# Optimization experiments

Hardware: AMD Instinct MI355X
Metric: run time of the kernel (lower is better)

## Reference

```python
import jax, jax.numpy as jnp
import numpy as np


def _conv3x3(x, w, b):
    # NCHW conv, stride 1, pad 1
    y = jax.lax.conv_general_dilated(x, w, (1, 1), ((1, 1), (1, 1)),
                                     dimension_numbers=('NCHW', 'OIHW', 'NCHW'))
    return y + b[None, :, None, None]


def _deform_conv3x3(x, offset, w):
    # Deformable conv v1: 3x3, stride 1, pad 1, 1 deformable group, no bias.
    # offset: [B, 18, H, W] laid out as (dy_k, dx_k) for k = 0..8 (row-major taps).
    B, C, H, W = x.shape
    K = 9
    off = offset.reshape(B, K, 2, H, W)
    ky, kx = jnp.meshgrid(jnp.arange(3), jnp.arange(3), indexing='ij')
    ky = (ky.reshape(K) - 1).astype(x.dtype)  # kernel tap y-offset, pad=1
    kx = (kx.reshape(K) - 1).astype(x.dtype)
    hh = jnp.arange(H, dtype=x.dtype)
    ww = jnp.arange(W, dtype=x.dtype)
    # sampling locations [B, K, H, W]
    sy = hh[None, None, :, None] + ky[None, :, None, None] + off[:, :, 0]
    sx = ww[None, None, None, :] + kx[None, :, None, None] + off[:, :, 1]
    y0 = jnp.floor(sy)
    x0 = jnp.floor(sx)
    ly = sy - y0  # fractional parts
    lx = sx - x0
    x_flat = x.reshape(B, C, H * W)

    def gather(yi, xi, wgt):
        # zero-padding semantics: corners outside the image contribute 0
        valid = (yi >= 0) & (yi < H) & (xi >= 0) & (xi < W)
        idx = (jnp.clip(yi, 0, H - 1).astype(jnp.int32) * W
               + jnp.clip(xi, 0, W - 1).astype(jnp.int32)).reshape(B, 1, K * H * W)
        v = jnp.take_along_axis(x_flat, idx, axis=2).reshape(B, C, K, H, W)
        return v * (wgt * valid.astype(x.dtype))[:, None]

    sampled = (gather(y0,     x0,     (1 - ly) * (1 - lx))
             + gather(y0,     x0 + 1, (1 - ly) * lx)
             + gather(y0 + 1, x0,     ly * (1 - lx))
             + gather(y0 + 1, x0 + 1, ly * lx))  # [B, C, K, H, W]
    return jnp.einsum('bckhw,ock->bohw', sampled, w.reshape(w.shape[0], C, K))


def setup_inputs() -> dict:
    key = jax.random.key(0)
    ks = jax.random.split(key, 8)
    C, O = 256, 256
    return {
        'kernel': jax.random.normal(ks[0], (16, C, 16, 16), jnp.float32),
        'search': jax.random.normal(ks[1], (16, C, 32, 32), jnp.float32),
        'Toffset_w': jax.random.normal(ks[2], (18, C, 3, 3), jnp.float32) * 0.02,
        'Toffset_b': jnp.zeros((18,), jnp.float32),
        'Tdeform_w': jax.random.normal(ks[3], (O, C, 3, 3), jnp.float32) * 0.02,
        'Soffset_w': jax.random.normal(ks[4], (18, C, 3, 3), jnp.float32) * 0.02,
        'Soffset_b': jnp.zeros((18,), jnp.float32),
        'Sdeform_w': jax.random.normal(ks[5], (O, C, 3, 3), jnp.float32) * 0.02,
    }


def reference(kernel, search, Toffset_w, Toffset_b, Tdeform_w,
              Soffset_w, Soffset_b, Sdeform_w):
    kernel_offset = _conv3x3(kernel, Toffset_w, Toffset_b)
    kernel_out = _deform_conv3x3(kernel, kernel_offset, Tdeform_w)
    search_offset = _conv3x3(search, Soffset_w, Soffset_b)
    search_out = _deform_conv3x3(search, search_offset, Sdeform_w)
    return (kernel_out, search_out, kernel_offset, search_offset)
```

## Files before the change

### kernel.cpp

```cpp
#include <hip/hip_runtime.h>

#define CIN   256
#define OC    256
#define K_TOT 2304
#define CCH   32
#define NCHK  8
#define KCH   288
#define SSTR  296
#define DM    64

#define N_DW  (OC * K_TOT)
#define N_OW  (32 * K_TOT)
#define N_CVT (2 * N_DW + 2 * N_OW)
#define CVT_BLOCKS (N_CVT / 4 / 256)

typedef short  bf16x8 __attribute__((ext_vector_type(8)));
typedef float  f32x4  __attribute__((ext_vector_type(4)));
typedef unsigned short ushort_t;

__device__ __forceinline__ ushort_t f2bf(float f) {
    unsigned u = __builtin_bit_cast(unsigned, f);
    u += 0x7fffu + ((u >> 16) & 1u);
    return (ushort_t)(u >> 16);
}
__device__ __forceinline__ float bf2f(short s) {
    return __builtin_bit_cast(float, ((unsigned)(unsigned short)s) << 16);
}

__global__ __launch_bounds__(256) void prep_k(
    const float* __restrict__ tdw, const float* __restrict__ sdw,
    const float* __restrict__ tow, const float* __restrict__ sow,
    const float* __restrict__ kin, const float* __restrict__ sin_,
    ushort_t* __restrict__ wk_d, ushort_t* __restrict__ ws_d,
    ushort_t* __restrict__ wk_o, ushort_t* __restrict__ ws_o,
    ushort_t* __restrict__ xt_k, ushort_t* __restrict__ xt_s)
{
    __shared__ ushort_t tile[64][264];

    if (blockIdx.x < CVT_BLOCKS) {
        const int i = (blockIdx.x * 256 + threadIdx.x) * 4;
        const float* src; ushort_t* dst; int j; bool offw = false;
        if (i < N_DW)                    { src = tdw; dst = wk_d; j = i; }
        else if (i < 2 * N_DW)           { src = sdw; dst = ws_d; j = i - N_DW; }
        else if (i < 2 * N_DW + N_OW)    { src = tow; dst = wk_o; j = i - 2 * N_DW; offw = true; }
        else                             { src = sow; dst = ws_o; j = i - 2 * N_DW - N_OW; offw = true; }
        const int oc = j / K_TOT;
        const int k  = j - oc * K_TOT;
        const int cc = k / KCH;
        const int r  = k - cc * KCH;
        const int tap = r >> 5;
        const int cl  = r & 31;
        ushort4 o4 = {0, 0, 0, 0};
        if (!offw || oc < 18) {
            const float* sp = &src[((size_t)oc * CIN + cc * 32 + cl) * 9 + tap];
            o4.x = f2bf(sp[0]); o4.y = f2bf(sp[9]); o4.z = f2bf(sp[18]); o4.w = f2bf(sp[27]);
        }
        *(ushort4*)&dst[j] = o4;
        return;
    }

    const int bx2 = blockIdx.x - CVT_BLOCKS;
    int H, W, b, px0; const float* x; ushort_t* xt;
    if (bx2 < 64) {
        H = 16; W = 16; x = kin; xt = xt_k;
        b = bx2 >> 2; px0 = (bx2 & 3) * 64;
    } else {
        int t2 = bx2 - 64;
        H = 32; W = 32; x = sin_; xt = xt_s;
        b = t2 >> 4; px0 = (t2 & 15) * 64;
    }
    const int HW = H * W;
    const int t = threadIdx.x, lane = t & 63, wv = t >> 6;
    const float* xb = x + (size_t)b * CIN * HW;

    for (int it = 0; it < 16; ++it) {
        const int ch = wv * 64 + it * 4 + (lane >> 4);
        const int pq = (lane & 15) * 4;
        float4 v = *(const float4*)&xb[(size_t)ch * HW + px0 + pq];
        tile[pq + 0][ch] = f2bf(v.x);
        tile[pq + 1][ch] = f2bf(v.y);
        tile[pq + 2][ch] = f2bf(v.z);
        tile[pq + 3][ch] = f2bf(v.w);
    }
    __syncthreads();
    for (int it = 0; it < 8; ++it) {
        const int px = it * 8 + wv * 2 + (lane >> 5);
        const int cg = (lane & 31) * 8;
        bf16x8 v = *(const bf16x8*)&tile[px][cg];
        *(bf16x8*)&xt[((size_t)b * HW + px0 + px) * 256 + cg] = v;
    }
}

__global__ __launch_bounds__(256, 2) void conv_gemm_k(
    const ushort_t* __restrict__ xt_k, const ushort_t* __restrict__ kwgt,
    const float* __restrict__ kbias, float* __restrict__ kout,
    const ushort_t* __restrict__ xt_s, const ushort_t* __restrict__ swgt,
    const float* __restrict__ sbias, float* __restrict__ sout)
{
    __shared__ float sred[3][4][2][64][4];

    int H, W, sh, b, px0;
    const ushort_t* xt; const ushort_t* wgt; const float* bias; float* out;
    if (blockIdx.x < 64) {
        H = 16; W = 16; sh = 4; xt = xt_k; wgt = kwgt; bias = kbias; out = kout;
        b = blockIdx.x >> 2; px0 = (blockIdx.x & 3) * 64;
    } else {
        int t2 = blockIdx.x - 64;
        H = 32; W = 32; sh = 5; xt = xt_s; wgt = swgt; bias = sbias; out = sout;
        b = t2 >> 4; px0 = (t2 & 15) * 64;
    }
    const int HW = H * W;
    const int t = threadIdx.x, lane = t & 63, kh = t >> 6;
    const int l15 = lane & 15;
    const int cg8 = (lane >> 4) * 8;
    const ushort_t* xtb = xt + (size_t)b * HW * 256;

    int h[4], wc[4];
#pragma unroll
    for (int mt = 0; mt < 4; ++mt) {
        const int px = px0 + mt * 16 + l15;
        h[mt]  = px >> sh;
        wc[mt] = px & (W - 1);
    }
    const ushort_t* wrow0 = wgt + (size_t)(l15)      * K_TOT + cg8;
    const ushort_t* wrow1 = wgt + (size_t)(16 + l15) * K_TOT + cg8;

    f32x4 acc[4][2] = {};
    for (int cc = kh * 2; cc < kh * 2 + 2; ++cc) {
        const int cb = cc * 32 + cg8;
#pragma unroll
        for (int ks = 0; ks < 9; ++ks) {
            const bf16x8 b0 = *(const bf16x8*)&wrow0[(size_t)cc * KCH + ks * 32];
            const bf16x8 b1 = *(const bf16x8*)&wrow1[(size_t)cc * KCH + ks * 32];
            const int dy = ks / 3 - 1, dx = ks % 3 - 1;
#pragma unroll
            for (int mt = 0; mt < 4; ++mt) {
                const int y  = h[mt] + dy;
                const int xx = wc[mt] + dx;
                const bool ok = ((unsigned)y < (unsigned)H) && ((unsigned)xx < (unsigned)W);
                bf16x8 a = {};
                if (ok) a = *(const bf16x8*)&xtb[(size_t)(((y << sh) + xx) * 256 + cb)];
                acc[mt][0] = __builtin_amdgcn_mfma_f32_16x16x32_bf16(a, b0, acc[mt][0], 0, 0, 0);
                acc[mt][1] = __builtin_amdgcn_mfma_f32_16x16x32_bf16(a, b1, acc[mt][1], 0, 0, 0);
            }
        }
    }

    if (kh > 0) {
#pragma unroll
        for (int mt = 0; mt < 4; ++mt)
#pragma unroll
            for (int nt = 0; nt < 2; ++nt)
                *(float4*)&sred[kh - 1][mt][nt][lane][0] = *(float4*)&acc[mt][nt];
    }
    __syncthreads();
    if (kh == 0) {
        const int prow = (lane >> 4) * 4;
#pragma unroll
        for (int nt = 0; nt < 2; ++nt) {
            const int oc = nt * 16 + l15;
            if (oc < 18) {
                const float bs = bias[oc];
#pragma unroll
                for (int mt = 0; mt < 4; ++mt) {
                    float4 r = *(float4*)&acc[mt][nt];
#pragma unroll
                    for (int q = 0; q < 3; ++q) {
                        const float4 o = *(const float4*)&sred[q][mt][nt][lane][0];
                        r.x += o.x; r.y += o.y; r.z += o.z; r.w += o.w;
                    }
                    r.x += bs; r.y += bs; r.z += bs; r.w += bs;
                    *(float4*)(out + ((size_t)b * 18 + oc) * HW + px0 + mt * 16 + prow) = r;
                }
            }
        }
    }
}

__device__ __forceinline__ void dcn_load4(
    bf16x8* c, const ushort_t* __restrict__ xtb, int4 id, int cb)
{
    c[0] = *(const bf16x8*)&xtb[(size_t)id.x * 256 + cb];
    c[1] = *(const bf16x8*)&xtb[(size_t)id.y * 256 + cb];
    c[2] = *(const bf16x8*)&xtb[(size_t)id.z * 256 + cb];
    c[3] = *(const bf16x8*)&xtb[(size_t)id.w * 256 + cb];
}
__device__ __forceinline__ void dcn_proc2(
    ushort_t* swb, int so, const bf16x8* c, float4 wt)
{
    bf16x8 r;
#pragma unroll
    for (int j = 0; j < 8; ++j) {
        const float v = wt.x * bf2f(c[0][j]) + wt.y * bf2f(c[1][j])
                      + wt.z * bf2f(c[2][j]) + wt.w * bf2f(c[3][j]);
        r[j] = (short)f2bf(v);
    }
    *(bf16x8*)&swb[so] = r;
}

__global__ __launch_bounds__(512, 4) void deform_gemm_k(
    const ushort_t* __restrict__ xt_k, const float* __restrict__ koffs,
    const ushort_t* __restrict__ kwgt, float* __restrict__ kout,
    const ushort_t* __restrict__ xt_s, const float* __restrict__ soffs,
    const ushort_t* __restrict__ swgt_, float* __restrict__ sout)
{
    __shared__ __align__(16) ushort_t smp[DM][SSTR];
    __shared__ __align__(16) int      sidx[DM][9][4];
    __shared__ __align__(16) float    swt [DM][9][4];

    int H, W, b, px0;
    const ushort_t* xt; const float* offs; const ushort_t* wgt; float* out;
    if (blockIdx.x < 64) {
        const int xcd = blockIdx.x & 7, i = blockIdx.x >> 3;
        H = 16; W = 16; xt = xt_k; offs = koffs; wgt = kwgt; out = kout;
        b = xcd + 8 * (i & 1); px0 = (i >> 1) * 64;
    } else {
        const int t2 = blockIdx.x - 64;
        const int xcd = t2 & 7, i = t2 >> 3;
        H = 32; W = 32; xt = xt_s; offs = soffs; wgt = swgt_; out = sout;
        b = xcd + 8 * (i & 1); px0 = (i >> 1) * 64;
    }
    const int HW = H * W;
    const int t = threadIdx.x, lane = t & 63, wv = t >> 6;

#pragma unroll
    for (int u = 0; u < 2; ++u) {
        const int s = t + u * 512;
        if (s < DM * 9) {
            const int p = s / 9, k = s - 9 * p;
            const int pix = px0 + p;
            const int h  = pix / W;
            const int wc = pix - h * W;
            const float* ob = offs + (size_t)b * 18 * HW;
            const float dy = ob[(2 * k    ) * HW + pix];
            const float dx = ob[(2 * k + 1) * HW + pix];
            const float sy = (float)(h  + k / 3 - 1) + dy;
            const float sx = (float)(wc + k % 3 - 1) + dx;
            const float y0f = floorf(sy), x0f = floorf(sx);
            const float ly = sy - y0f, lx = sx - x0f;
            const int y0 = (int)y0f, x0 = (int)x0f;
#pragma unroll
            for (int j = 0; j < 4; ++j) {
                const int yy = y0 + (j >> 1);
                const int xx = x0 + (j & 1);
                const bool ok = ((unsigned)yy < (unsigned)H) && ((unsigned)xx < (unsigned)W);
                sidx[p][k][j] = min(max(yy, 0), H - 1) * W + min(max(xx, 0), W - 1);
                const float wj = ((j >> 1) ? ly : 1.f - ly) * ((j & 1) ? lx : 1.f - lx);
                swt[p][k][j] = ok ? wj : 0.f;
            }
        }
    }
    __syncthreads();

    const ushort_t* xtb = xt + (size_t)b * HW * 256;
    const int l15 = lane & 15;
    const int cg8 = (lane >> 4) * 8;
    const int ocb = wv * 32;
    const bool live4 = (t < 256);

    const int g0  = t >> 2;
    const int cgE = (t & 3) * 8;
    int uso[5];
#pragma unroll
    for (int q = 0; q < 5; ++q) {
        const int g  = g0 + q * 128;
        const int px = g / 9, tap = g - 9 * px;
        uso[q] = px * SSTR + tap * 32 + (t & 3) * 8;
    }

    const ushort_t* wrow0 = wgt + (size_t)(ocb      + l15) * K_TOT + cg8;
    const ushort_t* wrow1 = wgt + (size_t)(ocb + 16 + l15) * K_TOT + cg8;
    ushort_t* smpb = &smp[0][0];
    const int4*   sidxF = (const int4*)  &sidx[0][0][0];
    const float4* swtF  = (const float4*)&swt [0][0][0];

    f32x4 acc[4][2] = {};

    for (int cc = 0; cc < NCHK; ++cc) {
        const int cb = cc * 32 + cgE;
        const size_t kg0 = (size_t)cc * KCH;

        bf16x8 cA[4], cB[4];
        float4 wA, wB;
        bf16x8 bq[2][2];
        { const int4 id = sidxF[g0];       wA = swtF[g0];       dcn_load4(cA, xtb, id, cb); }
        { const int4 id = sidxF[g0 + 128]; wB = swtF[g0 + 128]; dcn_load4(cB, xtb, id, cb); }
        bq[0][0] = *(const bf16x8*)&wrow0[kg0];
        bq[0][1] = *(const bf16x8*)&wrow1[kg0];

        dcn_proc2(smpb, uso[0], cA, wA);
        { const int4 id = sidxF[g0 + 256]; wA = swtF[g0 + 256]; dcn_load4(cA, xtb, id, cb); }
        dcn_proc2(smpb, uso[1], cB, wB);
        { const int4 id = sidxF[g0 + 384]; wB = swtF[g0 + 384]; dcn_load4(cB, xtb, id, cb); }
        dcn_proc2(smpb, uso[2], cA, wA);
        if (live4) { const int4 id = sidxF[g0 + 512]; wA = swtF[g0 + 512]; dcn_load4(cA, xtb, id, cb); }
        dcn_proc2(smpb, uso[3], cB, wB);
        if (live4) dcn_proc2(smpb, uso[4], cA, wA);

        asm volatile("s_waitcnt lgkmcnt(0)" ::: "memory");
        __builtin_amdgcn_sched_barrier(0);
        __builtin_amdgcn_s_barrier();
        __builtin_amdgcn_sched_barrier(0);

        __builtin_amdgcn_s_setprio(1);
#pragma unroll
        for (int ks = 0; ks < 9; ++ks) {
            if (ks < 8) {
                bq[(ks + 1) & 1][0] = *(const bf16x8*)&wrow0[kg0 + (size_t)(ks + 1) * 32];
                bq[(ks + 1) & 1][1] = *(const bf16x8*)&wrow1[kg0 + (size_t)(ks + 1) * 32];
            }
            bf16x8 a[4];
#pragma unroll
            for (int mt = 0; mt < 4; ++mt)
                a[mt] = *(const bf16x8*)&smp[mt * 16 + l15][ks * 32 + cg8];
#pragma unroll
            for (int mt = 0; mt < 4; ++mt) {
                acc[mt][0] = __builtin_amdgcn_mfma_f32_16x16x32_bf16(a[mt], bq[ks & 1][0], acc[mt][0], 0, 0, 0);
                acc[mt][1] = __builtin_amdgcn_mfma_f32_16x16x32_bf16(a[mt], bq[ks & 1][1], acc[mt][1], 0, 0, 0);
            }
        }
        __builtin_amdgcn_s_setprio(0);

        if (cc < NCHK - 1) {
            __builtin_amdgcn_sched_barrier(0);
            __builtin_amdgcn_s_barrier();
            __builtin_amdgcn_sched_barrier(0);
        }
    }

    const int prow = (lane >> 4) * 4;
#pragma unroll
    for (int mt = 0; mt < 4; ++mt) {
#pragma unroll
        for (int nt = 0; nt < 2; ++nt) {
            const int oc = ocb + nt * 16 + l15;
            float* op = out + ((size_t)b * OC + oc) * HW + px0 + mt * 16 + prow;
            *(float4*)op = *(float4*)&acc[mt][nt];
        }
    }
}

extern "C" void kernel_launch(void* const* d_in, const int* in_sizes, int n_in,
                              void* d_out, int out_size, void* d_ws, size_t ws_size,
                              hipStream_t stream) {
    const float* kin = (const float*)d_in[0];
    const float* sin_ = (const float*)d_in[1];
    const float* tow = (const float*)d_in[2];
    const float* tob = (const float*)d_in[3];
    const float* tdw = (const float*)d_in[4];
    const float* sow = (const float*)d_in[5];
    const float* sob = (const float*)d_in[6];
    const float* sdw = (const float*)d_in[7];

    float* out = (float*)d_out;
    float* out_k  = out;
    float* out_s  = out_k + (size_t)16 * 256 * 16 * 16;
    float* out_ko = out_s + (size_t)16 * 256 * 32 * 32;
    float* out_so = out_ko + (size_t)16 * 18 * 16 * 16;

    ushort_t* wk_d = (ushort_t*)d_ws;
    ushort_t* ws_d = wk_d + N_DW;
    ushort_t* wk_o = ws_d + N_DW;
    ushort_t* ws_o = wk_o + N_OW;
    ushort_t* xt_k = ws_o + N_OW;
    ushort_t* xt_s = xt_k + (size_t)16 * 256 * 256;

    prep_k<<<dim3(CVT_BLOCKS + 320), 256, 0, stream>>>(
        tdw, sdw, tow, sow, kin, sin_,
        wk_d, ws_d, wk_o, ws_o, xt_k, xt_s);

    conv_gemm_k<<<dim3(320), 256, 0, stream>>>(
        xt_k, wk_o, tob, out_ko, xt_s, ws_o, sob, out_so);

    deform_gemm_k<<<dim3(320), 512, 0, stream>>>(
        xt_k, out_ko, wk_d, out_k, xt_s, out_so, ws_d, out_s);
}
```

Measured before the change: 207.5 us.

## Split offset-conv K across 8 waves with branchless zero-row loads and XCD-aware mapping

The offset conv GEMM now runs 512 threads per block, so each of 8 waves handles one 32-channel chunk instead of two, and the partial sums are reduced through a larger shared buffer with a padded layout. Out-of-bounds taps now load from a zeroed 256-element row placed after xt_s instead of using a predicated load, which lets all four A loads be issued before the MFMAs. Blocks are remapped so consecutive block IDs spread batches across XCDs. This adds more wave parallelism and memory-level parallelism, at the cost of a bigger reduction step and more LDS.

```diff
diff --git a/kernel.cpp b/kernel.cpp
--- a/kernel.cpp
+++ b/kernel.cpp
@@ -13,6 +13,8 @@
 #define N_OW  (32 * K_TOT)
 #define N_CVT (2 * N_DW + 2 * N_OW)
 #define CVT_BLOCKS (N_CVT / 4 / 256)
+#define XT_K_ELEMS ((size_t)16 * 256 * 256)
+#define XT_S_ELEMS ((size_t)16 * 1024 * 256)
 
 typedef short  bf16x8 __attribute__((ext_vector_type(8)));
 typedef float  f32x4  __attribute__((ext_vector_type(4)));
@@ -36,6 +38,11 @@
     ushort_t* __restrict__ xt_k, ushort_t* __restrict__ xt_s)
 {
     __shared__ ushort_t tile[64][264];
+
+    if (blockIdx.x == 0 && threadIdx.x < 64) {
+        ushort4 z = {0, 0, 0, 0};
+        *(ushort4*)&xt_s[XT_S_ELEMS + (size_t)threadIdx.x * 4] = z;
+    }
 
     if (blockIdx.x < CVT_BLOCKS) {
         const int i = (blockIdx.x * 256 + threadIdx.x) * 4;
@@ -91,23 +98,27 @@
     }
 }
 
-__global__ __launch_bounds__(256, 2) void conv_gemm_k(
+__global__ __launch_bounds__(512, 2) void conv_gemm_k(
     const ushort_t* __restrict__ xt_k, const ushort_t* __restrict__ kwgt,
     const float* __restrict__ kbias, float* __restrict__ kout,
     const ushort_t* __restrict__ xt_s, const ushort_t* __restrict__ swgt,
     const float* __restrict__ sbias, float* __restrict__ sout)
 {
-    __shared__ float sred[3][4][2][64][4];
-
-    int H, W, sh, b, px0;
+    __shared__ float sred[7][64][36];
+
+    int H, W, sh, b, px0; int zrel;
     const ushort_t* xt; const ushort_t* wgt; const float* bias; float* out;
     if (blockIdx.x < 64) {
+        const int xcd = blockIdx.x & 7, i = blockIdx.x >> 3;
         H = 16; W = 16; sh = 4; xt = xt_k; wgt = kwgt; bias = kbias; out = kout;
-        b = blockIdx.x >> 2; px0 = (blockIdx.x & 3) * 64;
+        b = xcd + 8 * (i & 1); px0 = (i >> 1) * 64;
+        zrel = (int)(XT_K_ELEMS + XT_S_ELEMS - (size_t)b * 256 * 256);
     } else {
-        int t2 = blockIdx.x - 64;
+        const int t2 = blockIdx.x - 64;
+        const int xcd = t2 & 7, i = t2 >> 3;
         H = 32; W = 32; sh = 5; xt = xt_s; wgt = swgt; bias = sbias; out = sout;
-        b = t2 >> 4; px0 = (t2 & 15) * 64;
+        b = xcd + 8 * (i & 1); px0 = (i >> 1) * 64;
+        zrel = (int)(XT_S_ELEMS - (size_t)b * 1024 * 256);
     }
     const int HW = H * W;
     const int t = threadIdx.x, lane = t & 63, kh = t >> 6;
@@ -124,25 +135,28 @@
     }
     const ushort_t* wrow0 = wgt + (size_t)(l15)      * K_TOT + cg8;
     const ushort_t* wrow1 = wgt + (size_t)(16 + l15) * K_TOT + cg8;
+    const int cb = kh * 32 + cg8;
+    const size_t kg0 = (size_t)kh * KCH;
 
     f32x4 acc[4][2] = {};
-    for (int cc = kh * 2; cc < kh * 2 + 2; ++cc) {
-        const int cb = cc * 32 + cg8;
-#pragma unroll
-        for (int ks = 0; ks < 9; ++ks) {
-            const bf16x8 b0 = *(const bf16x8*)&wrow0[(size_t)cc * KCH + ks * 32];
-            const bf16x8 b1 = *(const bf16x8*)&wrow1[(size_t)cc * KCH + ks * 32];
-            const int dy = ks / 3 - 1, dx = ks % 3 - 1;
-#pragma unroll
-            for (int mt = 0; mt < 4; ++mt) {
-                const int y  = h[mt] + dy;
-                const int xx = wc[mt] + dx;
-                const bool ok = ((unsigned)y < (unsigned)H) && ((unsigned)xx < (unsigned)W);
-                bf16x8 a = {};
-                if (ok) a = *(const bf16x8*)&xtb[(size_t)(((y << sh) + xx) * 256 + cb)];
-                acc[mt][0] = __builtin_amdgcn_mfma_f32_16x16x32_bf16(a, b0, acc[mt][0], 0, 0, 0);
-                acc[mt][1] = __builtin_amdgcn_mfma_f32_16x16x32_bf16(a, b1, acc[mt][1], 0, 0, 0);
-            }
+#pragma unroll
+    for (int ks = 0; ks < 9; ++ks) {
+        const bf16x8 b0 = *(const bf16x8*)&wrow0[kg0 + (size_t)ks * 32];
+        const bf16x8 b1 = *(const bf16x8*)&wrow1[kg0 + (size_t)ks * 32];
+        const int dy = ks / 3 - 1, dx = ks % 3 - 1;
+        bf16x8 a[4];
+#pragma unroll
+        for (int mt = 0; mt < 4; ++mt) {
+            const int y  = h[mt] + dy;
+            const int xx = wc[mt] + dx;
+            const bool ok = ((unsigned)y < (unsigned)H) && ((unsigned)xx < (unsigned)W);
+            const int off = ok ? (((y << sh) + xx) * 256 + cb) : (zrel + cb);
+            a[mt] = *(const bf16x8*)&xtb[off];
+        }
+#pragma unroll
+        for (int mt = 0; mt < 4; ++mt) {
+            acc[mt][0] = __builtin_amdgcn_mfma_f32_16x16x32_bf16(a[mt], b0, acc[mt][0], 0, 0, 0);
+            acc[mt][1] = __builtin_amdgcn_mfma_f32_16x16x32_bf16(a[mt], b1, acc[mt][1], 0, 0, 0);
         }
     }
 
@@ -151,7 +165,7 @@
         for (int mt = 0; mt < 4; ++mt)
 #pragma unroll
             for (int nt = 0; nt < 2; ++nt)
-                *(float4*)&sred[kh - 1][mt][nt][lane][0] = *(float4*)&acc[mt][nt];
+                *(float4*)&sred[kh - 1][lane][(mt * 2 + nt) * 4] = *(float4*)&acc[mt][nt];
     }
     __syncthreads();
     if (kh == 0) {
@@ -165,8 +179,8 @@
                 for (int mt = 0; mt < 4; ++mt) {
                     float4 r = *(float4*)&acc[mt][nt];
 #pragma unroll
-                    for (int q = 0; q < 3; ++q) {
-                        const float4 o = *(const float4*)&sred[q][mt][nt][lane][0];
+                    for (int q = 0; q < 7; ++q) {
+                        const float4 o = *(const float4*)&sred[q][lane][(mt * 2 + nt) * 4];
                         r.x += o.x; r.y += o.y; r.z += o.z; r.w += o.w;
                     }
                     r.x += bs; r.y += bs; r.z += bs; r.w += bs;
@@ -363,13 +377,13 @@
     ushort_t* wk_o = ws_d + N_DW;
     ushort_t* ws_o = wk_o + N_OW;
     ushort_t* xt_k = ws_o + N_OW;
-    ushort_t* xt_s = xt_k + (size_t)16 * 256 * 256;
+    ushort_t* xt_s = xt_k + XT_K_ELEMS;
 
     prep_k<<<dim3(CVT_BLOCKS + 320), 256, 0, stream>>>(
         tdw, sdw, tow, sow, kin, sin_,
         wk_d, ws_d, wk_o, ws_o, xt_k, xt_s);
 
-    conv_gemm_k<<<dim3(320), 256, 0, stream>>>(
+    conv_gemm_k<<<dim3(320), 512, 0, stream>>>(
         xt_k, wk_o, tob, out_ko, xt_s, ws_o, sob, out_so);
 
     deform_gemm_k<<<dim3(320), 512, 0, stream>>>(
```

Result: no change. 208.0 us (+0.2%).
